# Kernel tuning notes

Measured on AMD Instinct MI355X. Metric: run time of the kernel, lower is better.

## Reference

```python
import jax, jax.numpy as jnp
import numpy as np

B, L, E, H, V, DT, C = 64, 80, 256, 256, 30000, 100, 4
D = 4 * L * H  # BatchNorm / FC feature dim = max_length * hidden * 4
EPS = 1e-5


def setup_inputs() -> dict:
    key = jax.random.key(0)
    ks = jax.random.split(key, 20)
    n = lambda k, shape, s: jax.random.normal(k, shape, jnp.float32) * s
    g = 1.0 / np.sqrt(H)  # pytorch LSTM init scale
    return {
        "arg1": jax.random.randint(ks[0], (B, L), 0, V, dtype=jnp.int32),
        "arg2": jax.random.randint(ks[1], (B, L), 0, V, dtype=jnp.int32),
        "seq_lengths": jnp.full((B,), L, dtype=jnp.int32),
        "transE1": jax.random.normal(ks[2], (L, DT), jnp.float32),
        "transE2": jax.random.normal(ks[3], (L, DT), jnp.float32),
        # learned parameters
        "table": n(ks[4], (V, E), 0.05),                 # embedding (xavier-ish)
        "Wih_f": n(ks[5], (4 * H, E), g),
        "Whh_f": n(ks[6], (4 * H, H), g),
        "bih_f": n(ks[7], (4 * H,), g),
        "bhh_f": n(ks[8], (4 * H,), g),
        "Wih_b": n(ks[9], (4 * H, E), g),
        "Whh_b": n(ks[10], (4 * H, H), g),
        "bih_b": n(ks[11], (4 * H,), g),
        "bhh_b": n(ks[12], (4 * H,), g),
        "R": jax.random.uniform(ks[13], (2 * E, 2 * E), jnp.float32),  # torch.rand init
        "gamma": jnp.ones((D,), jnp.float32),
        "beta": jnp.zeros((D,), jnp.float32),
        "fcW": n(ks[14], (C, D), 0.01),
        "fcb": jnp.zeros((C,), jnp.float32),
    }


def _lstm_dir(x, Wih, Whh, b):
    # x: (B, L, E); pytorch gate order i, f, g, o
    xg = jnp.einsum('ble,ge->blg', x, Wih) + b          # (B, L, 4H)
    xg = jnp.swapaxes(xg, 0, 1)                         # (L, B, 4H)
    h0 = jnp.zeros((x.shape[0], Whh.shape[1]), x.dtype)

    def step(carry, g_t):
        h, c = carry
        gates = g_t + h @ Whh.T
        i, f, gg, o = jnp.split(gates, 4, axis=-1)
        c = jax.nn.sigmoid(f) * c + jax.nn.sigmoid(i) * jnp.tanh(gg)
        h = jax.nn.sigmoid(o) * jnp.tanh(c)
        return (h, c), h

    _, hs = jax.lax.scan(step, (h0, h0), xg)
    return jnp.swapaxes(hs, 0, 1)                       # (B, L, H)


def _bilstm(x, Wih_f, Whh_f, bih_f, bhh_f, Wih_b, Whh_b, bih_b, bhh_b):
    fwd = _lstm_dir(x, Wih_f, Whh_f, bih_f + bhh_f)
    bwd = _lstm_dir(x[:, ::-1], Wih_b, Whh_b, bih_b + bhh_b)[:, ::-1]
    return jnp.concatenate([fwd, bwd], axis=-1)         # (B, L, 2H)


def _forward(arg1, arg2, transE1, transE2, table, Wih_f, Whh_f, bih_f, bhh_f,
             Wih_b, Whh_b, bih_b, bhh_b, R, gamma, beta, fcW, fcb):
    # deal_transE: relation[i,j] = tanh(mean(arg1_word_i - arg2_word_j));
    # identical for every batch element -> block-diagonal kron.
    m1 = transE1.mean(axis=1)                           # (L,)
    m2 = transE2.mean(axis=1)                           # (L,)
    rel = jnp.tanh(m1[:, None] - m2[None, :])           # (L, L)
    kg = jax.lax.stop_gradient(jnp.kron(jnp.eye(B, dtype=rel.dtype), rel))  # (B*L, B*L)

    e1 = table[arg1]                                    # (B, L, E); dropout p=0 -> identity
    e2 = table[arg2]
    o1 = _bilstm(e1, Wih_f, Whh_f, bih_f, bhh_f, Wih_b, Whh_b, bih_b, bhh_b)
    o2 = _bilstm(e2, Wih_f, Whh_f, bih_f, bhh_f, Wih_b, Whh_b, bih_b, bhh_b)

    N = B * L
    t1 = o1.reshape(N, 2 * H)
    t2 = o2.reshape(N, 2 * H)

    last = jnp.tanh((t1 @ R) @ t2.T) + kg               # (N, N)
    sf1 = jax.nn.softmax(last, axis=1).mean(axis=0)[:, None]  # (N, 1)
    sf2 = jax.nn.softmax(last, axis=0).mean(axis=1)[:, None]  # (N, 1)

    out1 = (t1 * sf2).reshape(B, L, 2 * H)
    out2 = (t2 * sf1).reshape(B, L, 2 * H)
    out = jnp.concatenate([out1, out2], axis=1).reshape(B, -1)  # (B, D)

    # BatchNorm1d in training mode (biased variance over batch)
    mu = out.mean(axis=0)
    var = out.var(axis=0)
    xn = (out - mu) / jnp.sqrt(var + EPS) * gamma + beta

    logits = xn @ fcW.T + fcb
    return jax.nn.log_softmax(logits, axis=1)           # (B, C)


def reference(arg1, arg2, seq_lengths, transE1, transE2, table, Wih_f, Whh_f,
              bih_f, bhh_f, Wih_b, Whh_b, bih_b, bhh_b, R, gamma, beta, fcW, fcb):
    del seq_lengths  # only encodes (B, L), which are static here
    return _forward(arg1, arg2, transE1, transE2, table, Wih_f, Whh_f, bih_f,
                    bhh_f, Wih_b, Whh_b, bih_b, bhh_b, R, gamma, beta, fcW, fcb)
```

## Files before the change

### kernel.cpp

```cpp
#include <hip/hip_runtime.h>
#include <cstddef>
#include <cstdint>

typedef unsigned short ushort_t;

constexpr int B_ = 64, L_ = 80, E_ = 256, H_ = 256, C_ = 4, DT_ = 100;
constexpr int N_ = B_ * L_;
constexpr int G4_ = 4 * H_;
constexpr int DH2_ = 2 * H_;
constexpr int DF_ = 4 * L_ * H_;
constexpr float EPS_ = 1e-5f;
constexpr int FB_USH = 32768;

typedef short s8v __attribute__((ext_vector_type(8)));
typedef float f4v __attribute__((ext_vector_type(4)));
typedef ushort_t us8 __attribute__((ext_vector_type(8)));

__device__ inline ushort_t f2bf_rn(float x) {
    uint32_t u = __builtin_bit_cast(uint32_t, x);
    uint32_t r = (u + 0x7fffu + ((u >> 16) & 1u)) >> 16;
    return (ushort_t)r;
}
__device__ inline float bf2f(ushort_t h) {
    uint32_t u = ((uint32_t)h) << 16;
    return __builtin_bit_cast(float, u);
}
__device__ inline float rcpf(float x) { return __builtin_amdgcn_rcpf(x); }
__device__ inline float sigm(float x) { return rcpf(1.f + __expf(-x)); }
__device__ inline float tanh_fast(float x) {
    float e2 = __expf(2.f * x);
    return 1.f - 2.f * rcpf(1.f + e2);
}

#define MFMA_B16(a, b, c) __builtin_amdgcn_mfma_f32_16x16x32_bf16((a), (b), (c), 0, 0, 0)

__global__ void k_rel(const float* __restrict__ tE1, const float* __restrict__ tE2,
                      float* __restrict__ rel) {
    __shared__ float m1[80], m2[80];
    int t = threadIdx.x;
    if (t < 80) {
        float s = 0.f;
        for (int k = 0; k < DT_; ++k) s += tE1[t * DT_ + k];
        m1[t] = s * (1.0f / DT_);
    } else if (t < 160) {
        int i = t - 80;
        float s = 0.f;
        for (int k = 0; k < DT_; ++k) s += tE2[i * DT_ + k];
        m2[i] = s * (1.0f / DT_);
    }
    __syncthreads();
    for (int idx = t; idx < 80 * 80; idx += blockDim.x)
        rel[idx] = tanhf(m1[idx / 80] - m2[idx % 80]);
}

__global__ void k_embed2(const int* __restrict__ arg1, const int* __restrict__ arg2,
                         const float* __restrict__ table,
                         ushort_t* __restrict__ ehi, ushort_t* __restrict__ elo) {
    int r = blockIdx.x;
    int rr = (r >= N_) ? (r - N_) : r;
    int idx = (r >= N_) ? arg2[rr] : arg1[rr];
    float v = table[(size_t)idx * E_ + threadIdx.x];
    ushort_t h = f2bf_rn(v);
    ehi[(size_t)r * E_ + threadIdx.x] = h;
    elo[(size_t)r * E_ + threadIdx.x] = f2bf_rn(v - bf2f(h));
}

__global__ void k_pack2(const float* __restrict__ Wih_f, const float* __restrict__ Wih_b,
                        const float* __restrict__ bih_f, const float* __restrict__ bhh_f,
                        const float* __restrict__ bih_b, const float* __restrict__ bhh_b,
                        const float* __restrict__ R,
                        ushort_t* __restrict__ Wchi, ushort_t* __restrict__ Wclo,
                        float* __restrict__ bcat,
                        ushort_t* __restrict__ Rthi, ushort_t* __restrict__ Rtlo) {
    int i = blockIdx.x * blockDim.x + threadIdx.x;
    if (i < 2 * G4_ * E_) {
        float v = (i < G4_ * E_) ? Wih_f[i] : Wih_b[i - G4_ * E_];
        ushort_t h = f2bf_rn(v);
        Wchi[i] = h;
        Wclo[i] = f2bf_rn(v - bf2f(h));
    }
    if (i < 2 * G4_)
        bcat[i] = (i < G4_) ? (bih_f[i] + bhh_f[i]) : (bih_b[i - G4_] + bhh_b[i - G4_]);
    if (i < 512 * 512) {
        int m = i >> 9, k = i & 511;
        float v = R[k * 512 + m];
        ushort_t h = f2bf_rn(v);
        Rthi[i] = h;
        Rtlo[i] = f2bf_rn(v - bf2f(h));
    }
}

__global__ void k_packw(const float* __restrict__ Whh_f, const float* __restrict__ Whh_b,
                        ushort_t* __restrict__ Bhi, ushort_t* __restrict__ Blo) {
    int idx = blockIdx.x * 256 + threadIdx.x;
    if (idx >= 2 * 16 * 8 * 4 * 64 * 8) return;
    int e = idx & 7;
    int lane = (idx >> 3) & 63;
    int g = (idx >> 9) & 3;
    int kt = (idx >> 11) & 7;
    int w = (idx >> 14) & 15;
    int d = idx >> 18;
    int c = lane & 15, q = lane >> 4;
    int row = g * 256 + w * 16 + c;
    int k = kt * 32 + q * 8 + e;
    const float* W = d ? Whh_b : Whh_f;
    float v = W[row * 256 + k];
    ushort_t hi = f2bf_rn(v);
    Bhi[idx] = hi;
    Blo[idx] = f2bf_rn(v - bf2f(hi));
}

__global__ void k_initlstm(ushort_t* __restrict__ fragbuf, int* __restrict__ flags) {
    int i = blockIdx.x * 256 + threadIdx.x;
    if (i < 64) flags[i] = 0;
    uint4* p = (uint4*)fragbuf;
    for (int jj = i; jj < 32768; jj += gridDim.x * 256)
        p[jj] = make_uint4(0u, 0u, 0u, 0u);
}

__global__ __launch_bounds__(1024, 4) void k_lstm8(
        const float* __restrict__ xg,
        const ushort_t* __restrict__ Bhi, const ushort_t* __restrict__ Blo,
        float* __restrict__ o1, float* __restrict__ o2,
        ushort_t* __restrict__ o1hi, ushort_t* __restrict__ o1lo,
        ushort_t* __restrict__ o2hi, ushort_t* __restrict__ o2lo,
        ushort_t* __restrict__ fragbuf, int* __restrict__ flags) {
    const int bid = blockIdx.x;
    const int s = bid & 15;
    const int Mh = (bid >> 4) & 1;
    const int d = bid >> 5;
    const int tid = threadIdx.x;
    const int w_id = tid >> 6, lane = tid & 63;
    const int g = w_id & 3, mt = w_id >> 2;
    const int c16 = lane & 15, qq = lane >> 4;

    __shared__ __align__(16) ushort_t Abuf[32768];
    __shared__ float pre[4][64][16];

    s8v bh[8], bl[8];
    {
        const s8v* BH = (const s8v*)Bhi;
        const s8v* BL = (const s8v*)Blo;
        int base = (d * 16 + s) * 2048 + g * 64 + lane;
        #pragma unroll
        for (int kt = 0; kt < 8; ++kt) {
            bh[kt] = BH[base + kt * 256];
            bl[kt] = BL[base + kt * 256];
        }
    }

    const int c_loc = tid >> 4, j = tid & 15;
    const int kglob = s * 16 + j;
    const int p_kt = kglob >> 5;
    const int p_q = (kglob & 31) >> 3, p_e = kglob & 7;
    const int p_lane = (c_loc & 15) | (p_q << 4);
    const int p_mt = c_loc >> 4;
    const int fb_off = ((p_mt * 8 + p_kt) * 64 + p_lane) * 8 + p_e;
    float* o_out = Mh ? o2 : o1;
    ushort_t* ophi = Mh ? o2hi : o1hi;
    ushort_t* oplo = Mh ? o2lo : o1lo;
    float cst = 0.f;

    const int grp = bid >> 4;
    const int* myflag = &flags[grp * 16 + w_id];
    const int kt_s = w_id >> 1;
    const int q0 = (w_id & 1) * 2;

    for (int t = 0; t < L_; ++t) {
        int l = d ? (L_ - 1 - t) : t;

        float xv[4];
        {
            const float* xp = xg + (size_t)(Mh * N_ + c_loc * L_ + l) * 2048
                              + d * 1024 + kglob;
            #pragma unroll
            for (int gg = 0; gg < 4; ++gg) xv[gg] = xp[gg * 256];
        }

        if (t > 0) {
            while (__hip_atomic_load(myflag, __ATOMIC_RELAXED,
                                     __HIP_MEMORY_SCOPE_AGENT) < t)
                __builtin_amdgcn_s_sleep(2);
        }
        {
            const ushort_t* fb = fragbuf
                + (size_t)((d * 2 + (t & 1)) * 2 + Mh) * FB_USH;
            #pragma unroll
            for (int ch = 0; ch < 8; ++ch) {
                int mtc = ch & 3, pl = ch >> 2;
                int off = pl * 16384 + ((mtc * 8 + kt_s) * 64 + q0 * 16) * 8 + lane * 4;
                unsigned long long v = __hip_atomic_load(
                    (const unsigned long long*)(fb + off), __ATOMIC_RELAXED,
                    __HIP_MEMORY_SCOPE_AGENT);
                *(unsigned long long*)&Abuf[off] = v;
            }
        }
        __syncthreads();

        f4v acc = {0.f, 0.f, 0.f, 0.f};
        {
            const s8v* AH = (const s8v*)&Abuf[0];
            const s8v* AL = (const s8v*)&Abuf[16384];
            #pragma unroll
            for (int kt = 0; kt < 8; ++kt) {
                s8v ah = AH[(mt * 8 + kt) * 64 + lane];
                s8v al = AL[(mt * 8 + kt) * 64 + lane];
                acc = MFMA_B16(ah, bh[kt], acc);
                acc = MFMA_B16(ah, bl[kt], acc);
                acc = MFMA_B16(al, bh[kt], acc);
            }
        }
        #pragma unroll
        for (int r = 0; r < 4; ++r)
            pre[g][mt * 16 + qq * 4 + r][c16] = acc[r];
        __syncthreads();

        float h;
        ushort_t hh, hl;
        size_t oidx;
        {
            float pi = pre[0][c_loc][j] + xv[0];
            float pf = pre[1][c_loc][j] + xv[1];
            float pg = pre[2][c_loc][j] + xv[2];
            float po = pre[3][c_loc][j] + xv[3];
            float si = sigm(pi), sf_ = sigm(pf), so = sigm(po);
            cst = sf_ * cst + si * tanh_fast(pg);
            h = so * tanh_fast(cst);
            oidx = (size_t)(c_loc * L_ + l) * DH2_ + d * H_ + kglob;
            hh = f2bf_rn(h);
            hl = f2bf_rn(h - bf2f(hh));
            ushort_t* fbn = fragbuf
                + (size_t)((d * 2 + ((t + 1) & 1)) * 2 + Mh) * FB_USH;
            __hip_atomic_store(&fbn[fb_off], hh, __ATOMIC_RELAXED,
                               __HIP_MEMORY_SCOPE_AGENT);
            __hip_atomic_store(&fbn[16384 + fb_off], hl, __ATOMIC_RELAXED,
                               __HIP_MEMORY_SCOPE_AGENT);
        }
        __syncthreads();

        if (tid == 0)
            __hip_atomic_store(&flags[bid], t + 1, __ATOMIC_RELAXED,
                               __HIP_MEMORY_SCOPE_AGENT);

        o_out[oidx] = h;
        ophi[oidx] = hh;
        oplo[oidx] = hl;
    }
}

__global__ __launch_bounds__(256) void k_gemm_bf(
        const ushort_t* __restrict__ Ahi, const ushort_t* __restrict__ Alo,
        const ushort_t* __restrict__ Bthi, const ushort_t* __restrict__ Btlo,
        const float* __restrict__ bias, float* __restrict__ Cout,
        ushort_t* __restrict__ Couthi, ushort_t* __restrict__ Coutlo,
        int M, int Nn, int K) {
    __shared__ ushort_t smpool[4][4096];
    const int tid = threadIdx.x;
    const int w = tid >> 6, lane = tid & 63;
    const int wr = w >> 1, wc = w & 1;
    const int c16 = lane & 15, q4 = lane >> 4;
    const int nbx = Nn >> 7;
    const int cpx = ((M >> 7) * nbx) >> 3;
    const int fid = blockIdx.x;
    const int swz = (fid & 7) * cpx + (fid >> 3);
    const int bx = swz % nbx, by = swz / nbx;
    const int r0 = by * 128, c0 = bx * 128;

    f4v acc[4][4] = {};
    const ushort_t* planes[4] = {
        Ahi + (size_t)r0 * K, Alo + (size_t)r0 * K,
        Bthi + (size_t)c0 * K, Btlo + (size_t)c0 * K };

    for (int kk = 0; kk < K; kk += 32) {
        #pragma unroll
        for (int p = 0; p < 4; ++p) {
            const ushort_t* src = planes[p] + kk;
            #pragma unroll
            for (int it = 0; it < 2; ++it) {
                int idx = it * 256 + tid;
                int row = idx >> 2, q = idx & 3;
                *(us8*)&smpool[p][(q * 128 + row) * 8] =
                    *(const us8*)&src[(size_t)row * K + q * 8];
            }
        }
        __syncthreads();
        s8v ah[4], al[4], bhv[4], blv[4];
        #pragma unroll
        for (int mi = 0; mi < 4; ++mi) {
            int ar = wr * 64 + mi * 16 + c16;
            ah[mi] = *(const s8v*)&smpool[0][(q4 * 128 + ar) * 8];
            al[mi] = *(const s8v*)&smpool[1][(q4 * 128 + ar) * 8];
        }
        #pragma unroll
        for (int ni = 0; ni < 4; ++ni) {
            int br = wc * 64 + ni * 16 + c16;
            bhv[ni] = *(const s8v*)&smpool[2][(q4 * 128 + br) * 8];
            blv[ni] = *(const s8v*)&smpool[3][(q4 * 128 + br) * 8];
        }
        #pragma unroll
        for (int mi = 0; mi < 4; ++mi)
            #pragma unroll
            for (int ni = 0; ni < 4; ++ni) {
                acc[mi][ni] = MFMA_B16(ah[mi], bhv[ni], acc[mi][ni]);
                acc[mi][ni] = MFMA_B16(ah[mi], blv[ni], acc[mi][ni]);
                acc[mi][ni] = MFMA_B16(al[mi], bhv[ni], acc[mi][ni]);
            }
        __syncthreads();
    }
    #pragma unroll
    for (int mi = 0; mi < 4; ++mi)
        #pragma unroll
        for (int rg = 0; rg < 4; ++rg) {
            int row = r0 + wr * 64 + mi * 16 + q4 * 4 + rg;
            #pragma unroll
            for (int ni = 0; ni < 4; ++ni) {
                int col = c0 + wc * 64 + ni * 16 + c16;
                float v = acc[mi][ni][rg] + (bias ? bias[col] : 0.f);
                size_t idx = (size_t)row * Nn + col;
                if (Couthi) {
                    ushort_t h = f2bf_rn(v);
                    Couthi[idx] = h;
                    Coutlo[idx] = f2bf_rn(v - bf2f(h));
                } else {
                    Cout[idx] = v;
                }
            }
        }
}

__global__ __launch_bounds__(256) void k_bigm(
        const ushort_t* __restrict__ uhi, const ushort_t* __restrict__ ulo,
        const ushort_t* __restrict__ vhi, const ushort_t* __restrict__ vlo,
        const float* __restrict__ rel, float* __restrict__ Ebuf,
        float* __restrict__ rowpart, float* __restrict__ colpart) {
    __shared__ ushort_t smpool[4][4096];
    const int tid = threadIdx.x;
    const int w = tid >> 6, lane = tid & 63;
    const int wr = w >> 1, wc = w & 1;
    const int c16 = lane & 15, q4 = lane >> 4;
    const int fid = blockIdx.x;
    const int swz = (fid & 7) * 200 + (fid >> 3);
    const int bx = swz % 40, by = swz / 40;
    const int r0 = by * 128, c0 = bx * 128;

    f4v acc[4][4] = {};
    const ushort_t* planes[4] = {
        uhi + (size_t)r0 * DH2_, ulo + (size_t)r0 * DH2_,
        vhi + (size_t)c0 * DH2_, vlo + (size_t)c0 * DH2_ };

    for (int kk = 0; kk < 16; ++kk) {
        #pragma unroll
        for (int p = 0; p < 4; ++p) {
            const ushort_t* src = planes[p] + kk * 32;
            #pragma unroll
            for (int it = 0; it < 2; ++it) {
                int idx = it * 256 + tid;
                int row = idx >> 2, q = idx & 3;
                *(us8*)&smpool[p][(q * 128 + row) * 8] =
                    *(const us8*)&src[(size_t)row * DH2_ + q * 8];
            }
        }
        __syncthreads();
        s8v ah[4], al[4], bhv[4], blv[4];
        #pragma unroll
        for (int mi = 0; mi < 4; ++mi) {
            int ar = wr * 64 + mi * 16 + c16;
            ah[mi] = *(const s8v*)&smpool[0][(q4 * 128 + ar) * 8];
            al[mi] = *(const s8v*)&smpool[1][(q4 * 128 + ar) * 8];
        }
        #pragma unroll
        for (int ni = 0; ni < 4; ++ni) {
            int br = wc * 64 + ni * 16 + c16;
            bhv[ni] = *(const s8v*)&smpool[2][(q4 * 128 + br) * 8];
            blv[ni] = *(const s8v*)&smpool[3][(q4 * 128 + br) * 8];
        }
        #pragma unroll
        for (int mi = 0; mi < 4; ++mi)
            #pragma unroll
            for (int ni = 0; ni < 4; ++ni) {
                acc[mi][ni] = MFMA_B16(ah[mi], bhv[ni], acc[mi][ni]);
                acc[mi][ni] = MFMA_B16(ah[mi], blv[ni], acc[mi][ni]);
                acc[mi][ni] = MFMA_B16(al[mi], bhv[ni], acc[mi][ni]);
            }
        __syncthreads();
    }

    float* rowred = (float*)&smpool[0][0];
    float* colred = rowred + 128 * 32;

    int gcolv[4], bjv[4], ljv[4];
    #pragma unroll
    for (int ni = 0; ni < 4; ++ni) {
        int coll = wc * 64 + ni * 16 + c16;
        gcolv[ni] = c0 + coll;
        bjv[ni] = gcolv[ni] / 80;
        ljv[ni] = gcolv[ni] - bjv[ni] * 80;
    }
    float csumv[4] = {0.f, 0.f, 0.f, 0.f};
    #pragma unroll
    for (int mi = 0; mi < 4; ++mi) {
        #pragma unroll
        for (int rg = 0; rg < 4; ++rg) {
            int rowl = wr * 64 + mi * 16 + q4 * 4 + rg;
            int grow = r0 + rowl;
            int bi = grow / 80, li = grow - bi * 80;
            float rsum = 0.f;
            #pragma unroll
            for (int ni = 0; ni < 4; ++ni) {
                float v = tanhf(acc[mi][ni][rg]);
                if (bi == bjv[ni]) v += rel[li * 80 + ljv[ni]];
                float ev = __expf(v);
                Ebuf[(size_t)grow * N_ + gcolv[ni]] = ev;
                rsum += ev;
                csumv[ni] += ev;
            }
            rowred[rowl * 32 + wc * 16 + c16] = rsum;
        }
    }
    #pragma unroll
    for (int ni = 0; ni < 4; ++ni) {
        int coll = wc * 64 + ni * 16 + c16;
        colred[coll * 8 + wr * 4 + q4] = csumv[ni];
    }
    __syncthreads();
    if (tid < 128) {
        float ssum = 0.f;
        #pragma unroll
        for (int t = 0; t < 32; ++t) ssum += rowred[tid * 32 + t];
        rowpart[(size_t)bx * N_ + r0 + tid] = ssum;
    } else {
        int c = tid - 128;
        float ssum = 0.f;
        #pragma unroll
        for (int t = 0; t < 8; ++t) ssum += colred[c * 8 + t];
        colpart[(size_t)by * N_ + c0 + c] = ssum;
    }
}

__global__ void k_redsum(const float* __restrict__ rowpart, const float* __restrict__ colpart,
                         float* __restrict__ rowinv, float* __restrict__ colinv) {
    int i = blockIdx.x * blockDim.x + threadIdx.x;
    if (i < N_) {
        float rs = 0.f, cs = 0.f;
        for (int t = 0; t < 40; ++t) {
            rs += rowpart[(size_t)t * N_ + i];
            cs += colpart[(size_t)t * N_ + i];
        }
        rowinv[i] = 1.f / rs;
        colinv[i] = 1.f / cs;
    }
}

__global__ __launch_bounds__(256) void k_sf2(const float* __restrict__ Ebuf,
                                             const float* __restrict__ colinv,
                                             float* __restrict__ sf2) {
    int i = blockIdx.x;
    float p = 0.f;
    for (int jj = threadIdx.x; jj < N_; jj += 256)
        p += Ebuf[(size_t)i * N_ + jj] * colinv[jj];
    __shared__ float red[256];
    red[threadIdx.x] = p;
    __syncthreads();
    for (int ss = 128; ss > 0; ss >>= 1) {
        if (threadIdx.x < ss) red[threadIdx.x] += red[threadIdx.x + ss];
        __syncthreads();
    }
    if (threadIdx.x == 0) sf2[i] = red[0] * (1.f / N_);
}

__global__ __launch_bounds__(256) void k_sf1part(const float* __restrict__ Ebuf,
                                                 const float* __restrict__ rowinv,
                                                 float* __restrict__ sf1part) {
    int col = blockIdx.x * 256 + threadIdx.x;
    int rc = blockIdx.y;
    float acc = 0.f;
    int r0 = rc * 320;
    for (int ii = 0; ii < 320; ++ii) {
        int row = r0 + ii;
        acc += Ebuf[(size_t)row * N_ + col] * rowinv[row];
    }
    sf1part[(size_t)rc * N_ + col] = acc;
}

__global__ void k_sf1red(const float* __restrict__ sf1part, float* __restrict__ sf1) {
    int jj = blockIdx.x * blockDim.x + threadIdx.x;
    if (jj < N_) {
        float s = 0.f;
        for (int t = 0; t < 16; ++t) s += sf1part[(size_t)t * N_ + jj];
        sf1[jj] = s * (1.f / N_);
    }
}

__global__ void k_bnstats(const float* __restrict__ o1, const float* __restrict__ o2,
                          const float* __restrict__ sf1, const float* __restrict__ sf2,
                          float* __restrict__ bnmu, float* __restrict__ bnrstd) {
    int f = blockIdx.x * 256 + threadIdx.x;
    int seg = f / (L_ * DH2_);
    int rem = f - seg * (L_ * DH2_);
    int l = rem >> 9, hh = rem & 511;
    const float* t = seg ? o2 : o1;
    const float* sf = seg ? sf1 : sf2;
    float s = 0.f, s2 = 0.f;
    for (int b = 0; b < B_; ++b) {
        int row = b * L_ + l;
        float x = t[(size_t)row * DH2_ + hh] * sf[row];
        s += x;
        s2 += x * x;
    }
    float mu = s * (1.f / B_);
    float v = fmaxf(s2 * (1.f / B_) - mu * mu, 0.f);
    bnmu[f] = mu;
    bnrstd[f] = rsqrtf(v + EPS_);
}

__global__ __launch_bounds__(256) void k_logits1(
        const float* __restrict__ o1, const float* __restrict__ o2,
        const float* __restrict__ sf1, const float* __restrict__ sf2,
        const float* __restrict__ bnmu, const float* __restrict__ bnrstd,
        const float* __restrict__ gamma, const float* __restrict__ beta,
        const float* __restrict__ fcW, float* __restrict__ part) {
    int b = blockIdx.x, ch = blockIdx.y;
    int tid = threadIdx.x;
    int f0 = ch * (DF_ / 5);
    float acc[4] = {0.f, 0.f, 0.f, 0.f};
    for (int f = f0 + tid; f < f0 + DF_ / 5; f += 256) {
        int seg = f / (L_ * DH2_);
        int rem = f - seg * (L_ * DH2_);
        int l = rem >> 9, hh = rem & 511;
        int row = b * L_ + l;
        float val = (seg ? o2 : o1)[(size_t)row * DH2_ + hh] * (seg ? sf1 : sf2)[row];
        float xn = (val - bnmu[f]) * bnrstd[f] * gamma[f] + beta[f];
        #pragma unroll
        for (int c = 0; c < 4; ++c) acc[c] += xn * fcW[(size_t)c * DF_ + f];
    }
    __shared__ float red[4][257];
    #pragma unroll
    for (int c = 0; c < 4; ++c) red[c][tid] = acc[c];
    __syncthreads();
    for (int ss = 128; ss > 0; ss >>= 1) {
        if (tid < ss)
            #pragma unroll
            for (int c = 0; c < 4; ++c) red[c][tid] += red[c][tid + ss];
        __syncthreads();
    }
    if (tid < 4) part[((size_t)b * 5 + ch) * 4 + tid] = red[tid][0];
}

__global__ void k_logits2(const float* __restrict__ part,
                          const float* __restrict__ fcb,
                          float* __restrict__ dout) {
    int b = blockIdx.x;
    if (threadIdx.x == 0) {
        float lg[4], mx = -1e30f;
        #pragma unroll
        for (int c = 0; c < 4; ++c) {
            float v = fcb[c];
            for (int ch = 0; ch < 5; ++ch) v += part[((size_t)b * 5 + ch) * 4 + c];
            lg[c] = v;
            mx = fmaxf(mx, v);
        }
        float se = 0.f;
        #pragma unroll
        for (int c = 0; c < 4; ++c) se += expf(lg[c] - mx);
        float lse = mx + logf(se);
        #pragma unroll
        for (int c = 0; c < 4; ++c) dout[b * 4 + c] = lg[c] - lse;
    }
}

extern "C" void kernel_launch(void* const* d_in, const int* in_sizes, int n_in,
                              void* d_out, int out_size, void* d_ws, size_t ws_size,
                              hipStream_t stream) {
    const int* arg1 = (const int*)d_in[0];
    const int* arg2 = (const int*)d_in[1];
    const float* tE1 = (const float*)d_in[3];
    const float* tE2 = (const float*)d_in[4];
    const float* table = (const float*)d_in[5];
    const float* Wih_f = (const float*)d_in[6];
    const float* Whh_f = (const float*)d_in[7];
    const float* bih_f = (const float*)d_in[8];
    const float* bhh_f = (const float*)d_in[9];
    const float* Wih_b = (const float*)d_in[10];
    const float* Whh_b = (const float*)d_in[11];
    const float* bih_b = (const float*)d_in[12];
    const float* bhh_b = (const float*)d_in[13];
    const float* R = (const float*)d_in[14];
    const float* gamma = (const float*)d_in[15];
    const float* beta = (const float*)d_in[16];
    const float* fcW = (const float*)d_in[17];
    const float* fcb = (const float*)d_in[18];
    float* dout = (float*)d_out;

    float* ws = (float*)d_ws;
    size_t off = 0;
    auto alloc = [&](size_t n) { float* p = ws + off; off += n; return p; };

    constexpr size_t PL = (size_t)N_ * DH2_;

    float* rel = alloc(80 * 80);
    float* eplanes = alloc((size_t)2 * N_ * E_);
    float* Wcplanes = alloc((size_t)2 * G4_ * E_);
    float* bcat = alloc(2 * G4_);
    float* Rtplanes = alloc((size_t)262144);
    float* o1 = alloc(PL);
    float* o2 = alloc(PL);
    float* planesA = alloc(PL);
    float* planesU = alloc(PL);
    float* rowpart = alloc((size_t)40 * N_);
    float* colpart = alloc((size_t)40 * N_);
    float* rowinv = alloc(N_);
    float* colinv = alloc(N_);
    float* sf1part = alloc((size_t)16 * N_);
    float* sf1 = alloc(N_);
    float* sf2 = alloc(N_);
    float* bnmu = alloc(DF_);
    float* bnrstd = alloc(DF_);
    float* lgpart = alloc((size_t)B_ * 5 * 4);
    ushort_t* Bhi = (ushort_t*)alloc(262144);
    ushort_t* Blo = (ushort_t*)alloc(262144);
    ushort_t* fragbuf = (ushort_t*)alloc(131072);
    int* flags = (int*)alloc(64);
    float* xg = alloc((size_t)N_ * N_);
    float* Ebuf = xg;

    ushort_t* ehi = (ushort_t*)eplanes;
    ushort_t* elo = ehi + (size_t)2 * N_ * E_;
    ushort_t* Wchi = (ushort_t*)Wcplanes;
    ushort_t* Wclo = Wchi + (size_t)2 * G4_ * E_;
    ushort_t* Rthi = (ushort_t*)Rtplanes;
    ushort_t* Rtlo = Rthi + 512 * 512;
    ushort_t* o1hi = (ushort_t*)planesA;
    ushort_t* o1lo = o1hi + PL;
    ushort_t* uhi = (ushort_t*)planesU;
    ushort_t* ulo = uhi + PL;
    ushort_t* o2hi = ehi;
    ushort_t* o2lo = elo;

    k_rel<<<1, 256, 0, stream>>>(tE1, tE2, rel);
    k_embed2<<<2 * N_, 256, 0, stream>>>(arg1, arg2, table, ehi, elo);
    k_pack2<<<2048, 256, 0, stream>>>(Wih_f, Wih_b, bih_f, bhh_f, bih_b, bhh_b, R,
                                      Wchi, Wclo, bcat, Rthi, Rtlo);
    k_packw<<<2048, 256, 0, stream>>>(Whh_f, Whh_b, Bhi, Blo);
    k_initlstm<<<64, 256, 0, stream>>>(fragbuf, flags);
    k_gemm_bf<<<1280, 256, 0, stream>>>(
        ehi, elo, Wchi, Wclo, bcat, xg, nullptr, nullptr, 2 * N_, 2048, E_);
    k_lstm8<<<64, 1024, 0, stream>>>(xg, Bhi, Blo, o1, o2,
                                     o1hi, o1lo, o2hi, o2lo, fragbuf, flags);
    k_gemm_bf<<<160, 256, 0, stream>>>(
        o1hi, o1lo, Rthi, Rtlo, nullptr, nullptr, uhi, ulo, N_, 512, 512);
    k_bigm<<<1600, 256, 0, stream>>>(
        uhi, ulo, o2hi, o2lo, rel, Ebuf, rowpart, colpart);
    k_redsum<<<(N_ + 255) / 256, 256, 0, stream>>>(rowpart, colpart, rowinv, colinv);
    k_sf2<<<N_, 256, 0, stream>>>(Ebuf, colinv, sf2);
    k_sf1part<<<dim3(20, 16), 256, 0, stream>>>(Ebuf, rowinv, sf1part);
    k_sf1red<<<(N_ + 255) / 256, 256, 0, stream>>>(sf1part, sf1);
    k_bnstats<<<DF_ / 256, 256, 0, stream>>>(o1, o2, sf1, sf2, bnmu, bnrstd);
    k_logits1<<<dim3(B_, 5), 256, 0, stream>>>(o1, o2, sf1, sf2, bnmu, bnrstd,
                                               gamma, beta, fcW, lgpart);
    k_logits2<<<B_, 64, 0, stream>>>(lgpart, fcb, dout);
}
```

Before: 757.2 us.

## Split LSTM recurrence across 256 smaller blocks with per-group flag sync

```diff
diff --git a/kernel.cpp b/kernel.cpp
--- a/kernel.cpp
+++ b/kernel.cpp
@@ -10,7 +10,7 @@
 constexpr int DH2_ = 2 * H_;
 constexpr int DF_ = 4 * L_ * H_;
 constexpr float EPS_ = 1e-5f;
-constexpr int FB_USH = 32768;
+constexpr int FB_USH = 8192;
 
 typedef short s8v __attribute__((ext_vector_type(8)));
 typedef float f4v __attribute__((ext_vector_type(4)));
@@ -112,13 +112,13 @@
 
 __global__ void k_initlstm(ushort_t* __restrict__ fragbuf, int* __restrict__ flags) {
     int i = blockIdx.x * 256 + threadIdx.x;
-    if (i < 64) flags[i] = 0;
+    if (i < 256) flags[i] = 0;
     uint4* p = (uint4*)fragbuf;
     for (int jj = i; jj < 32768; jj += gridDim.x * 256)
         p[jj] = make_uint4(0u, 0u, 0u, 0u);
 }
 
-__global__ __launch_bounds__(1024, 4) void k_lstm8(
+__global__ __launch_bounds__(256, 2) void k_lstm9(
         const float* __restrict__ xg,
         const ushort_t* __restrict__ Bhi, const ushort_t* __restrict__ Blo,
         float* __restrict__ o1, float* __restrict__ o2,
@@ -127,15 +127,14 @@
         ushort_t* __restrict__ fragbuf, int* __restrict__ flags) {
     const int bid = blockIdx.x;
     const int s = bid & 15;
-    const int Mh = (bid >> 4) & 1;
-    const int d = bid >> 5;
+    const int cg = (bid >> 4) & 7;
+    const int d = bid >> 7;
     const int tid = threadIdx.x;
-    const int w_id = tid >> 6, lane = tid & 63;
-    const int g = w_id & 3, mt = w_id >> 2;
+    const int g = tid >> 6, lane = tid & 63;
     const int c16 = lane & 15, qq = lane >> 4;
 
-    __shared__ __align__(16) ushort_t Abuf[32768];
-    __shared__ float pre[4][64][16];
+    __shared__ __align__(16) ushort_t Abuf[8192];
+    __shared__ float pre[4][16][16];
 
     s8v bh[8], bl[8];
     {
@@ -153,58 +152,59 @@
     const int kglob = s * 16 + j;
     const int p_kt = kglob >> 5;
     const int p_q = (kglob & 31) >> 3, p_e = kglob & 7;
-    const int p_lane = (c_loc & 15) | (p_q << 4);
-    const int p_mt = c_loc >> 4;
-    const int fb_off = ((p_mt * 8 + p_kt) * 64 + p_lane) * 8 + p_e;
-    float* o_out = Mh ? o2 : o1;
-    ushort_t* ophi = Mh ? o2hi : o1hi;
-    ushort_t* oplo = Mh ? o2lo : o1lo;
+    const int p_lane = c_loc | (p_q << 4);
+    const int fb_off = (p_kt * 64 + p_lane) * 8 + p_e;
+    const int cc = cg * 16 + c_loc;
+    const int w = cc >> 6, bb = cc & 63;
+    float* o_out = w ? o2 : o1;
+    ushort_t* ophi = w ? o2hi : o1hi;
+    ushort_t* oplo = w ? o2lo : o1lo;
     float cst = 0.f;
 
     const int grp = bid >> 4;
-    const int* myflag = &flags[grp * 16 + w_id];
-    const int kt_s = w_id >> 1;
-    const int q0 = (w_id & 1) * 2;
+    int* gflags = flags + grp * 16;
+    const size_t fbbase = (size_t)grp * 2 * FB_USH;
 
     for (int t = 0; t < L_; ++t) {
         int l = d ? (L_ - 1 - t) : t;
 
         float xv[4];
         {
-            const float* xp = xg + (size_t)(Mh * N_ + c_loc * L_ + l) * 2048
+            const float* xp = xg + (size_t)(w * N_ + bb * L_ + l) * 2048
                               + d * 1024 + kglob;
             #pragma unroll
             for (int gg = 0; gg < 4; ++gg) xv[gg] = xp[gg * 256];
         }
 
         if (t > 0) {
-            while (__hip_atomic_load(myflag, __ATOMIC_RELAXED,
-                                     __HIP_MEMORY_SCOPE_AGENT) < t)
-                __builtin_amdgcn_s_sleep(2);
-        }
+            if (tid < 16) {
+                while (__hip_atomic_load(&gflags[tid], __ATOMIC_RELAXED,
+                                         __HIP_MEMORY_SCOPE_AGENT) < t)
+                    __builtin_amdgcn_s_sleep(2);
+            }
+            __syncthreads();
+        }
+
         {
-            const ushort_t* fb = fragbuf
-                + (size_t)((d * 2 + (t & 1)) * 2 + Mh) * FB_USH;
-            #pragma unroll
-            for (int ch = 0; ch < 8; ++ch) {
-                int mtc = ch & 3, pl = ch >> 2;
-                int off = pl * 16384 + ((mtc * 8 + kt_s) * 64 + q0 * 16) * 8 + lane * 4;
-                unsigned long long v = __hip_atomic_load(
-                    (const unsigned long long*)(fb + off), __ATOMIC_RELAXED,
+            const unsigned long long* src = (const unsigned long long*)(fragbuf
+                + fbbase + (size_t)(t & 1) * FB_USH);
+            unsigned long long* dst = (unsigned long long*)Abuf;
+            #pragma unroll
+            for (int r = 0; r < 8; ++r)
+                dst[r * 256 + tid] = __hip_atomic_load(
+                    &src[r * 256 + tid], __ATOMIC_RELAXED,
                     __HIP_MEMORY_SCOPE_AGENT);
-                *(unsigned long long*)&Abuf[off] = v;
-            }
         }
         __syncthreads();
 
         f4v acc = {0.f, 0.f, 0.f, 0.f};
         {
             const s8v* AH = (const s8v*)&Abuf[0];
-            const s8v* AL = (const s8v*)&Abuf[16384];
+            const s8v* AL = (const s8v*)&Abuf[4096];
             #pragma unroll
             for (int kt = 0; kt < 8; ++kt) {
-                s8v ah = AH[(mt * 8 + kt) * 64 + lane];
-                s8v al = AL[(mt * 8 + kt) * 64 + lane];
+                s8v ah = AH[kt * 64 + lane];
+                s8v al = AL[kt * 64 + lane];
                 acc = MFMA_B16(ah, bh[kt], acc);
                 acc = MFMA_B16(ah, bl[kt], acc);
                 acc = MFMA_B16(al, bh[kt], acc);
@@ -212,7 +212,7 @@
         }
         #pragma unroll
         for (int r = 0; r < 4; ++r)
-            pre[g][mt * 16 + qq * 4 + r][c16] = acc[r];
+            pre[g][qq * 4 + r][c16] = acc[r];
         __syncthreads();
 
         float h;
@@ -226,14 +226,13 @@
             float si = sigm(pi), sf_ = sigm(pf), so = sigm(po);
             cst = sf_ * cst + si * tanh_fast(pg);
             h = so * tanh_fast(cst);
-            oidx = (size_t)(c_loc * L_ + l) * DH2_ + d * H_ + kglob;
+            oidx = (size_t)(bb * L_ + l) * DH2_ + d * H_ + kglob;
             hh = f2bf_rn(h);
             hl = f2bf_rn(h - bf2f(hh));
-            ushort_t* fbn = fragbuf
-                + (size_t)((d * 2 + ((t + 1) & 1)) * 2 + Mh) * FB_USH;
+            ushort_t* fbn = fragbuf + fbbase + (size_t)((t + 1) & 1) * FB_USH;
             __hip_atomic_store(&fbn[fb_off], hh, __ATOMIC_RELAXED,
                                __HIP_MEMORY_SCOPE_AGENT);
-            __hip_atomic_store(&fbn[16384 + fb_off], hl, __ATOMIC_RELAXED,
+            __hip_atomic_store(&fbn[4096 + fb_off], hl, __ATOMIC_RELAXED,
                                __HIP_MEMORY_SCOPE_AGENT);
         }
         __syncthreads();
@@ -619,7 +618,7 @@
     ushort_t* Bhi = (ushort_t*)alloc(262144);
     ushort_t* Blo = (ushort_t*)alloc(262144);
     ushort_t* fragbuf = (ushort_t*)alloc(131072);
-    int* flags = (int*)alloc(64);
+    int* flags = (int*)alloc(256);
     float* xg = alloc((size_t)N_ * N_);
     float* Ebuf = xg;
 
@@ -644,7 +643,7 @@
     k_initlstm<<<64, 256, 0, stream>>>(fragbuf, flags);
     k_gemm_bf<<<1280, 256, 0, stream>>>(
         ehi, elo, Wchi, Wclo, bcat, xg, nullptr, nullptr, 2 * N_, 2048, E_);
-    k_lstm8<<<64, 1024, 0, stream>>>(xg, Bhi, Blo, o1, o2,
+    k_lstm9<<<256, 256, 0, stream>>>(xg, Bhi, Blo, o1, o2,
                                      o1hi, o1lo, o2hi, o2lo, fragbuf, flags);
     k_gemm_bf<<<160, 256, 0, stream>>>(
         o1hi, o1lo, Rthi, Rtlo, nullptr, nullptr, uhi, ulo, N_, 512, 512);
```

New measurement: 639.0 us. -15.6%, faster.
